# Kernel optimization log

Hardware: AMD Instinct MI355X
Metric: run time of the kernel (lower is better)

Reference implementation:

```python
import jax, jax.numpy as jnp
import numpy as np

FEAT = 256      # config.feature_size
HID = 256       # config.hidden_size
MAXC = 10       # config.max_child_num
NSEM = 64       # Tree.num_sem
B = 32768       # number of parent nodes (one batched tree level)


def _forward(box_input, eps, W_box, b_box, W1, b1, W2, b2,
             Ws1, bs1, Wmu, bmu, Wvar, bvar, sem_ids, n_children):
    # ---- BoxEncoder on every leaf child: relu(Linear(10 -> FEAT)) ----
    leaf = jax.nn.relu(jnp.einsum('bmi,if->bmf', box_input, W_box) + b_box)  # [B,M,FEAT]
    # ---- concat semantic one-hot per child ----
    sem = jax.nn.one_hot(sem_ids, NSEM, dtype=leaf.dtype)                    # [B,M,NSEM]
    child_feats = jnp.concatenate([leaf, sem], axis=-1)                      # [B,M,FEAT+NSEM]
    # ---- SymmetricChildEncoder ----
    feat = jax.nn.relu(jnp.einsum('bmf,fh->bmh', child_feats, W1) + b1)      # [B,M,HID]
    exists = (jnp.arange(MAXC) < n_children[:, None]).astype(feat.dtype)[..., None]  # [B,M,1]
    x = jnp.max(feat * exists, axis=1)                                       # [B,HID]
    parent_feat = jax.nn.relu(x @ W2 + b2)                                   # [B,FEAT]
    # ---- Sampler (variational, probabilistic) ----
    enc = jax.nn.relu(parent_feat @ Ws1 + bs1)                               # [B,HID]
    mu = enc @ Wmu + bmu                                                     # [B,FEAT]
    logvar = enc @ Wvar + bvar                                               # [B,FEAT]
    std = jnp.exp(0.5 * logvar)
    kld = 1.0 + logvar - mu * mu - jnp.exp(logvar)
    return jnp.concatenate([eps * std + mu, kld], axis=1)                    # [B,2*FEAT]


def setup_inputs() -> dict:
    key = jax.random.key(0)
    ks = jax.random.split(key, 16)
    def lin_w(k, fan_in, shape):
        return (jax.random.normal(k, shape, jnp.float32) / np.sqrt(fan_in)).astype(jnp.float32)
    return {
        'box_input': jax.random.normal(ks[0], (B, MAXC, 10), jnp.float32),
        'eps': jax.random.normal(ks[1], (B, FEAT), jnp.float32),
        'W_box': lin_w(ks[2], 10, (10, FEAT)),
        'b_box': jnp.zeros((FEAT,), jnp.float32),
        'W1': lin_w(ks[3], FEAT + NSEM, (FEAT + NSEM, HID)),
        'b1': jnp.zeros((HID,), jnp.float32),
        'W2': lin_w(ks[4], HID, (HID, FEAT)),
        'b2': jnp.zeros((FEAT,), jnp.float32),
        'Ws1': lin_w(ks[5], FEAT, (FEAT, HID)),
        'bs1': jnp.zeros((HID,), jnp.float32),
        'Wmu': lin_w(ks[6], HID, (HID, FEAT)),
        'bmu': jnp.zeros((FEAT,), jnp.float32),
        'Wvar': lin_w(ks[7], HID, (HID, FEAT)),
        'bvar': jnp.zeros((FEAT,), jnp.float32),
        'sem_ids': jax.random.randint(ks[8], (B, MAXC), 0, NSEM, jnp.int32),
        'n_children': jax.random.randint(ks[9], (B,), 1, MAXC + 1, jnp.int32),
    }


def reference(box_input, eps, W_box, b_box, W1, b1, W2, b2,
              Ws1, bs1, Wmu, bmu, Wvar, bvar, sem_ids, n_children):
    return _forward(box_input, eps, W_box, b_box, W1, b1, W2, b2,
                    Ws1, bs1, Wmu, bmu, Wvar, bvar, sem_ids, n_children)
```

## Files before the change

kernel.cpp:

```cpp
#include <hip/hip_runtime.h>
#include <math.h>


#define NPAR  32768
#define LDA1  328
#define LDA2  264
#define W1F_OFF   0
#define W2F_OFF   81920
#define WBX_OFF   (81920 + 4*65536)
#define XBUF_OFF  (WBX_OFF + 8192)

typedef _Float16 f16;
typedef _Float16 f16x8 __attribute__((ext_vector_type(8)));
typedef float    f32x4 __attribute__((ext_vector_type(4)));

__device__ __forceinline__ void async16(const void* g, void* l) {
    __builtin_amdgcn_global_load_lds((const __attribute__((address_space(1))) void*)g,
                                     (__attribute__((address_space(3))) void*)l, 16, 0, 0);
}
__device__ __forceinline__ f32x4 mfma16(f16x8 a, f16x8 b, f32x4 c) {
    return __builtin_amdgcn_mfma_f32_16x16x32_f16(a, b, c, 0, 0, 0);
}

__global__ void kconv(const float* __restrict__ W1, const float* __restrict__ W2,
                      const float* __restrict__ Ws1, const float* __restrict__ Wmu,
                      const float* __restrict__ Wvar, const float* __restrict__ Wbox,
                      f16* __restrict__ ws) {
    int idx = blockIdx.x * 256 + threadIdx.x;
    if (idx < 81920) {
        int j = idx & 7, lane = (idx >> 3) & 63, t = idx >> 9;
        int c = t % 10, n16 = t / 10;
        int k = c * 32 + (lane >> 4) * 8 + j;
        int n = n16 * 16 + (lane & 15);
        ws[idx] = (f16)W1[k * 256 + n];
    } else if (idx < WBX_OFF) {
        int r = idx - 81920;
        int wsel = r >> 16, r2 = r & 65535;
        const float* s = (wsel == 0) ? W2 : (wsel == 1) ? Ws1 : (wsel == 2) ? Wmu : Wvar;
        int j = r2 & 7, lane = (r2 >> 3) & 63, c = (r2 >> 9) & 7, n16 = r2 >> 12;
        int k = c * 32 + (lane >> 4) * 8 + j;
        int n = n16 * 16 + (lane & 15);
        ws[idx] = (f16)s[k * 256 + n];
    } else if (idx < XBUF_OFF) {
        int r = idx - WBX_OFF;
        int j = r & 7, lane = (r >> 3) & 63, n16 = r >> 9;
        int k = (lane >> 4) * 8 + j;
        int n = n16 * 16 + (lane & 15);
        ws[idx] = (f16)((k < 10) ? Wbox[k * 256 + n] : 0.f);
    }
}

__global__ __launch_bounds__(256, 2)
void k1(const float* __restrict__ box, const float* __restrict__ bbox,
        const float* __restrict__ b1, const int* __restrict__ sem,
        const int* __restrict__ nch, const f16* __restrict__ wsh,
        f16* __restrict__ xbuf) {
    __shared__ __align__(16) f16 lA[80 * LDA1];
    __shared__ int lnc[8];

    int tid = threadIdx.x, blk = blockIdx.x;
    int w = tid >> 6, lane = tid & 63, q = lane >> 4, r16 = lane & 15;
    const f16* w1f = wsh + W1F_OFF;
    const f16* wbxf = wsh + WBX_OFF;

    if (tid < 8) lnc[tid] = nch[blk * 8 + tid];

    float bbv[4], b1v[4];
    #pragma unroll
    for (int nt = 0; nt < 4; nt++) {
        int col = w * 64 + nt * 16 + r16;
        bbv[nt] = bbox[col];
        b1v[nt] = b1[col];
    }

    f32x4 acc[5][4];
    {
        f16x8 bb[4], ab[5];
        #pragma unroll
        for (int nt = 0; nt < 4; nt++)
            bb[nt] = *(const f16x8*)&wbxf[((w * 4 + nt) * 64 + lane) * 8];
        #pragma unroll
        for (int mt = 0; mt < 5; mt++) {
            const float* bp = box + (size_t)blk * 800 + (mt * 16 + r16) * 10;
            float v[8] = {0.f, 0.f, 0.f, 0.f, 0.f, 0.f, 0.f, 0.f};
            if (q == 0) {
                float2 t0 = *(const float2*)(bp + 0), t1 = *(const float2*)(bp + 2);
                float2 t2 = *(const float2*)(bp + 4), t3 = *(const float2*)(bp + 6);
                v[0] = t0.x; v[1] = t0.y; v[2] = t1.x; v[3] = t1.y;
                v[4] = t2.x; v[5] = t2.y; v[6] = t3.x; v[7] = t3.y;
            } else if (q == 1) {
                float2 t = *(const float2*)(bp + 8);
                v[0] = t.x; v[1] = t.y;
            }
            f16x8 t;
            #pragma unroll
            for (int j = 0; j < 8; j++) t[j] = (f16)v[j];
            ab[mt] = t;
        }
        #pragma unroll
        for (int mt = 0; mt < 5; mt++)
            #pragma unroll
            for (int nt = 0; nt < 4; nt++)
                acc[mt][nt] = mfma16(ab[mt], bb[nt], (f32x4){0.f, 0.f, 0.f, 0.f});
    }
    #pragma unroll
    for (int mt = 0; mt < 5; mt++) {
        #pragma unroll
        for (int i = 0; i < 4; i++) {
            int r = mt * 16 + q * 4 + i;
            int p = (r * 205) >> 11;
            int d = (r - 10 * p) * 8 + p;
            #pragma unroll
            for (int nt = 0; nt < 4; nt++) {
                int col = w * 64 + nt * 16 + r16;
                lA[d * LDA1 + col] = (f16)fmaxf(acc[mt][nt][i] + bbv[nt], 0.f);
            }
        }
    }
    if (tid < 80) {
        int p8 = tid & 7, m8 = tid >> 3;
        int sid = sem[blk * 80 + p8 * 10 + m8];
        f16x8 z = {(f16)0.f, (f16)0.f, (f16)0.f, (f16)0.f, (f16)0.f, (f16)0.f, (f16)0.f, (f16)0.f};
        #pragma unroll
        for (int j = 0; j < 8; j++) *(f16x8*)&lA[tid * LDA1 + 256 + j * 8] = z;
        lA[tid * LDA1 + 256 + sid] = (f16)1.f;
    }

    #pragma unroll
    for (int mt = 0; mt < 5; mt++)
        #pragma unroll
        for (int nt = 0; nt < 4; nt++) acc[mt][nt] = (f32x4){0.f, 0.f, 0.f, 0.f};

    f16x8 bs[3][4];
    auto loadB = [&](int c, int s) {
        #pragma unroll
        for (int nt = 0; nt < 4; nt++)
            bs[s][nt] = *(const f16x8*)&w1f[(((w * 4 + nt) * 10 + c) * 64 + lane) * 8];
    };
    loadB(0, 0); loadB(1, 1); loadB(2, 2);
    __syncthreads();
    #pragma unroll
    for (int c = 0; c < 10; c++) {
        f16x8 a[5];
        #pragma unroll
        for (int mt = 0; mt < 5; mt++)
            a[mt] = *(const f16x8*)&lA[(mt * 16 + r16) * LDA1 + c * 32 + q * 8];
        int s = c % 3;
        #pragma unroll
        for (int mt = 0; mt < 5; mt++)
            #pragma unroll
            for (int nt = 0; nt < 4; nt++) acc[mt][nt] = mfma16(a[mt], bs[s][nt], acc[mt][nt]);
        if (c + 3 < 10) loadB(c + 3, s);
    }

    int qh = q >> 1, qb = q & 1;
    int ncv[4];
    #pragma unroll
    for (int i = 0; i < 4; i++) ncv[i] = lnc[4 * qb + i];
    float pm[4][4];
    #pragma unroll
    for (int i = 0; i < 4; i++)
        #pragma unroll
        for (int nt = 0; nt < 4; nt++) pm[i][nt] = 0.f;
    #pragma unroll
    for (int mt = 0; mt < 5; mt++) {
        int m = 2 * mt + qh;
        #pragma unroll
        for (int i = 0; i < 4; i++) {
            bool live = m < ncv[i];
            #pragma unroll
            for (int nt = 0; nt < 4; nt++) {
                float v = fmaxf(acc[mt][nt][i] + b1v[nt], 0.f);
                pm[i][nt] = fmaxf(pm[i][nt], live ? v : 0.f);
            }
        }
    }
    #pragma unroll
    for (int i = 0; i < 4; i++)
        #pragma unroll
        for (int nt = 0; nt < 4; nt++)
            pm[i][nt] = fmaxf(pm[i][nt], __shfl_xor(pm[i][nt], 32, 64));
    if (q < 2) {
        #pragma unroll
        for (int i = 0; i < 4; i++) {
            size_t row = (size_t)blk * 8 + 4 * q + i;
            #pragma unroll
            for (int nt = 0; nt < 4; nt++)
                xbuf[row * LDA2 + w * 64 + nt * 16 + r16] = (f16)pm[i][nt];
        }
    }
}

__global__ __launch_bounds__(256, 2)
void k2(const f16* __restrict__ xbuf, const f16* __restrict__ wsh,
        const float* __restrict__ b2, const float* __restrict__ bs1,
        const float* __restrict__ bmu, const float* __restrict__ bvar,
        const float* __restrict__ eps, float* __restrict__ out) {
    __shared__ __align__(16) f16 actA[32 * LDA2];
    __shared__ __align__(16) f16 actB[32 * LDA2];

    int tid = threadIdx.x, blk = blockIdx.x;
    int w = tid >> 6, lane = tid & 63, q = lane >> 4, r16 = lane & 15;
    const f16* w2f   = wsh + W2F_OFF;
    const f16* ws1f  = w2f + 65536;
    const f16* wmuf  = w2f + 2 * 65536;
    const f16* wvarf = w2f + 3 * 65536;

    float b2v[4], bs1v[4], bmv[4], bvv[4];
    #pragma unroll
    for (int nt = 0; nt < 4; nt++) {
        int col = w * 64 + nt * 16 + r16;
        b2v[nt] = b2[col]; bs1v[nt] = bs1[col];
        bmv[nt] = bmu[col]; bvv[nt] = bvar[col];
    }

    {
        const char* src = (const char*)(xbuf + (size_t)blk * 32 * LDA2);
        #pragma unroll
        for (int j = 0; j < 5; j++) {
            int idx = tid + j * 256;
            if (idx < 1056) async16(src + idx * 16, (char*)actA + idx * 16);
        }
    }

    f32x4 acc[2][4];
    f16x8 bs[3][4];
    auto loadB = [&](const f16* wt, int c, int s) {
        #pragma unroll
        for (int nt = 0; nt < 4; nt++)
            bs[s][nt] = *(const f16x8*)&wt[(((w * 4 + nt) * 8 + c) * 64 + lane) * 8];
    };
    auto gemm = [&](const f16* A, const f16* wt) {
        #pragma unroll
        for (int mt = 0; mt < 2; mt++)
            #pragma unroll
            for (int nt = 0; nt < 4; nt++) acc[mt][nt] = (f32x4){0.f, 0.f, 0.f, 0.f};
        #pragma unroll
        for (int c = 0; c < 8; c++) {
            f16x8 a[2];
            #pragma unroll
            for (int mt = 0; mt < 2; mt++)
                a[mt] = *(const f16x8*)&A[(mt * 16 + r16) * LDA2 + c * 32 + q * 8];
            int s = c % 3;
            #pragma unroll
            for (int mt = 0; mt < 2; mt++)
                #pragma unroll
                for (int nt = 0; nt < 4; nt++) acc[mt][nt] = mfma16(a[mt], bs[s][nt], acc[mt][nt]);
            if (c + 3 < 8) loadB(wt, c + 3, s);
        }
    };

    loadB(w2f, 0, 0); loadB(w2f, 1, 1); loadB(w2f, 2, 2);
    __syncthreads();
    gemm(actA, w2f);
    #pragma unroll
    for (int nt = 0; nt < 4; nt++) {
        int col = w * 64 + nt * 16 + r16;
        #pragma unroll
        for (int mt = 0; mt < 2; mt++)
            #pragma unroll
            for (int i = 0; i < 4; i++)
                actB[(mt * 16 + q * 4 + i) * LDA2 + col] = (f16)fmaxf(acc[mt][nt][i] + b2v[nt], 0.f);
    }
    loadB(ws1f, 0, 0); loadB(ws1f, 1, 1); loadB(ws1f, 2, 2);
    __syncthreads();

    gemm(actB, ws1f);
    #pragma unroll
    for (int nt = 0; nt < 4; nt++) {
        int col = w * 64 + nt * 16 + r16;
        #pragma unroll
        for (int mt = 0; mt < 2; mt++)
            #pragma unroll
            for (int i = 0; i < 4; i++)
                actA[(mt * 16 + q * 4 + i) * LDA2 + col] = (f16)fmaxf(acc[mt][nt][i] + bs1v[nt], 0.f);
    }
    loadB(wmuf, 0, 0); loadB(wmuf, 1, 1); loadB(wmuf, 2, 2);
    __syncthreads();

    gemm(actA, wmuf);
    f32x4 mu[2][4];
    #pragma unroll
    for (int mt = 0; mt < 2; mt++)
        #pragma unroll
        for (int nt = 0; nt < 4; nt++) mu[mt][nt] = acc[mt][nt];

    float ev[2][4][4];
    #pragma unroll
    for (int mt = 0; mt < 2; mt++)
        #pragma unroll
        for (int i = 0; i < 4; i++) {
            size_t grow = (size_t)blk * 32 + mt * 16 + q * 4 + i;
            #pragma unroll
            for (int nt = 0; nt < 4; nt++)
                ev[mt][nt][i] = eps[grow * 256 + w * 64 + nt * 16 + r16];
        }

    loadB(wvarf, 0, 0); loadB(wvarf, 1, 1); loadB(wvarf, 2, 2);
    gemm(actA, wvarf);
    #pragma unroll
    for (int mt = 0; mt < 2; mt++)
        #pragma unroll
        for (int nt = 0; nt < 4; nt++) {
            int col = w * 64 + nt * 16 + r16;
            #pragma unroll
            for (int i = 0; i < 4; i++) {
                size_t grow = (size_t)blk * 32 + mt * 16 + q * 4 + i;
                float m_ = mu[mt][nt][i] + bmv[nt];
                float lv = acc[mt][nt][i] + bvv[nt];
                float e  = expf(lv);
                out[grow * 512 + col]       = ev[mt][nt][i] * sqrtf(e) + m_;
                out[grow * 512 + 256 + col] = 1.f + lv - m_ * m_ - e;
            }
        }
}

extern "C" void kernel_launch(void* const* d_in, const int* in_sizes, int n_in,
                              void* d_out, int out_size, void* d_ws, size_t ws_size,
                              hipStream_t stream) {
    const float* box  = (const float*)d_in[0];
    const float* eps  = (const float*)d_in[1];
    const float* Wbox = (const float*)d_in[2];
    const float* bbox = (const float*)d_in[3];
    const float* W1   = (const float*)d_in[4];
    const float* b1   = (const float*)d_in[5];
    const float* W2   = (const float*)d_in[6];
    const float* b2   = (const float*)d_in[7];
    const float* Ws1  = (const float*)d_in[8];
    const float* bs1  = (const float*)d_in[9];
    const float* Wmu  = (const float*)d_in[10];
    const float* bmu  = (const float*)d_in[11];
    const float* Wvar = (const float*)d_in[12];
    const float* bvar = (const float*)d_in[13];
    const int*   sem  = (const int*)d_in[14];
    const int*   nch  = (const int*)d_in[15];

    f16* wsh  = (f16*)d_ws;
    f16* xbuf = wsh + XBUF_OFF;

    kconv<<<XBUF_OFF / 256, 256, 0, stream>>>(W1, W2, Ws1, Wmu, Wvar, Wbox, wsh);
    k1<<<NPAR / 8, 256, 0, stream>>>(box, bbox, b1, sem, nch, wsh, xbuf);
    k2<<<NPAR / 32, 256, 0, stream>>>(xbuf, wsh, b2, bs1, bmu, bvar, eps, (float*)d_out);
}
```

Baseline: 218.8 us.

## Fuse child-encoder and sampler kernels, keep pooled features in LDS

Merges the two main kernels into one. Each block now loops over four 8-parent groups to build a 32-row pooled feature tile in shared memory, then runs the W2/Ws1/Wmu/Wvar GEMM chain on that tile directly. This removes the global xbuf round trip and one kernel launch. In exchange it cuts the grid to a quarter of the former k1 block count, serialises the four groups inside a block, and raises LDS use per block, which may lower occupancy.

```diff
diff --git a/kernel.cpp b/kernel.cpp
--- a/kernel.cpp
+++ b/kernel.cpp
@@ -8,16 +8,12 @@
 #define W1F_OFF   0
 #define W2F_OFF   81920
 #define WBX_OFF   (81920 + 4*65536)
-#define XBUF_OFF  (WBX_OFF + 8192)
+#define WS_END    (WBX_OFF + 8192)
 
 typedef _Float16 f16;
 typedef _Float16 f16x8 __attribute__((ext_vector_type(8)));
 typedef float    f32x4 __attribute__((ext_vector_type(4)));
 
-__device__ __forceinline__ void async16(const void* g, void* l) {
-    __builtin_amdgcn_global_load_lds((const __attribute__((address_space(1))) void*)g,
-                                     (__attribute__((address_space(3))) void*)l, 16, 0, 0);
-}
 __device__ __forceinline__ f32x4 mfma16(f16x8 a, f16x8 b, f32x4 c) {
     return __builtin_amdgcn_mfma_f32_16x16x32_f16(a, b, c, 0, 0, 0);
 }
@@ -41,7 +37,7 @@
         int k = c * 32 + (lane >> 4) * 8 + j;
         int n = n16 * 16 + (lane & 15);
         ws[idx] = (f16)s[k * 256 + n];
-    } else if (idx < XBUF_OFF) {
+    } else if (idx < WS_END) {
         int r = idx - WBX_OFF;
         int j = r & 7, lane = (r >> 3) & 63, n16 = r >> 9;
         int k = (lane >> 4) * 8 + j;
@@ -51,19 +47,20 @@
 }
 
 __global__ __launch_bounds__(256, 2)
-void k1(const float* __restrict__ box, const float* __restrict__ bbox,
+void kf(const float* __restrict__ box, const float* __restrict__ bbox,
         const float* __restrict__ b1, const int* __restrict__ sem,
         const int* __restrict__ nch, const f16* __restrict__ wsh,
-        f16* __restrict__ xbuf) {
+        const float* __restrict__ b2, const float* __restrict__ bs1,
+        const float* __restrict__ bmu, const float* __restrict__ bvar,
+        const float* __restrict__ eps, float* __restrict__ out) {
     __shared__ __align__(16) f16 lA[80 * LDA1];
+    __shared__ __align__(16) f16 xl[32 * LDA2];
     __shared__ int lnc[8];
 
     int tid = threadIdx.x, blk = blockIdx.x;
     int w = tid >> 6, lane = tid & 63, q = lane >> 4, r16 = lane & 15;
-    const f16* w1f = wsh + W1F_OFF;
+    const f16* w1f  = wsh + W1F_OFF;
     const f16* wbxf = wsh + WBX_OFF;
-
-    if (tid < 8) lnc[tid] = nch[blk * 8 + tid];
 
     float bbv[4], b1v[4];
     #pragma unroll
@@ -73,138 +70,137 @@
         b1v[nt] = b1[col];
     }
 
-    f32x4 acc[5][4];
-    {
-        f16x8 bb[4], ab[5];
-        #pragma unroll
-        for (int nt = 0; nt < 4; nt++)
-            bb[nt] = *(const f16x8*)&wbxf[((w * 4 + nt) * 64 + lane) * 8];
+    #pragma unroll 1
+    for (int t = 0; t < 4; t++) {
+        int g = blk * 4 + t;
+        if (t) __syncthreads();
+
+        if (tid < 8) lnc[tid] = nch[g * 8 + tid];
+
+        f32x4 acc[5][4];
+        {
+            f16x8 bb[4], ab[5];
+            #pragma unroll
+            for (int nt = 0; nt < 4; nt++)
+                bb[nt] = *(const f16x8*)&wbxf[((w * 4 + nt) * 64 + lane) * 8];
+            #pragma unroll
+            for (int mt = 0; mt < 5; mt++) {
+                const float* bp = box + (size_t)g * 800 + (mt * 16 + r16) * 10;
+                float v[8] = {0.f, 0.f, 0.f, 0.f, 0.f, 0.f, 0.f, 0.f};
+                if (q == 0) {
+                    float2 t0 = *(const float2*)(bp + 0), t1 = *(const float2*)(bp + 2);
+                    float2 t2 = *(const float2*)(bp + 4), t3 = *(const float2*)(bp + 6);
+                    v[0] = t0.x; v[1] = t0.y; v[2] = t1.x; v[3] = t1.y;
+                    v[4] = t2.x; v[5] = t2.y; v[6] = t3.x; v[7] = t3.y;
+                } else if (q == 1) {
+                    float2 tt = *(const float2*)(bp + 8);
+                    v[0] = tt.x; v[1] = tt.y;
+                }
+                f16x8 tv;
+                #pragma unroll
+                for (int j = 0; j < 8; j++) tv[j] = (f16)v[j];
+                ab[mt] = tv;
+            }
+            #pragma unroll
+            for (int mt = 0; mt < 5; mt++)
+                #pragma unroll
+                for (int nt = 0; nt < 4; nt++)
+                    acc[mt][nt] = mfma16(ab[mt], bb[nt], (f32x4){0.f, 0.f, 0.f, 0.f});
+        }
         #pragma unroll
         for (int mt = 0; mt < 5; mt++) {
-            const float* bp = box + (size_t)blk * 800 + (mt * 16 + r16) * 10;
-            float v[8] = {0.f, 0.f, 0.f, 0.f, 0.f, 0.f, 0.f, 0.f};
-            if (q == 0) {
-                float2 t0 = *(const float2*)(bp + 0), t1 = *(const float2*)(bp + 2);
-                float2 t2 = *(const float2*)(bp + 4), t3 = *(const float2*)(bp + 6);
-                v[0] = t0.x; v[1] = t0.y; v[2] = t1.x; v[3] = t1.y;
-                v[4] = t2.x; v[5] = t2.y; v[6] = t3.x; v[7] = t3.y;
-            } else if (q == 1) {
-                float2 t = *(const float2*)(bp + 8);
-                v[0] = t.x; v[1] = t.y;
-            }
-            f16x8 t;
-            #pragma unroll
-            for (int j = 0; j < 8; j++) t[j] = (f16)v[j];
-            ab[mt] = t;
-        }
+            #pragma unroll
+            for (int i = 0; i < 4; i++) {
+                int r = mt * 16 + q * 4 + i;
+                int p = (r * 205) >> 11;
+                int d = (r - 10 * p) * 8 + p;
+                #pragma unroll
+                for (int nt = 0; nt < 4; nt++) {
+                    int col = w * 64 + nt * 16 + r16;
+                    lA[d * LDA1 + col] = (f16)fmaxf(acc[mt][nt][i] + bbv[nt], 0.f);
+                }
+            }
+        }
+        if (tid < 80) {
+            int p8 = tid & 7, m8 = tid >> 3;
+            int sid = sem[g * 80 + p8 * 10 + m8];
+            f16x8 z = {(f16)0.f, (f16)0.f, (f16)0.f, (f16)0.f, (f16)0.f, (f16)0.f, (f16)0.f, (f16)0.f};
+            #pragma unroll
+            for (int j = 0; j < 8; j++) *(f16x8*)&lA[tid * LDA1 + 256 + j * 8] = z;
+            lA[tid * LDA1 + 256 + sid] = (f16)1.f;
+        }
+
         #pragma unroll
         for (int mt = 0; mt < 5; mt++)
             #pragma unroll
+            for (int nt = 0; nt < 4; nt++) acc[mt][nt] = (f32x4){0.f, 0.f, 0.f, 0.f};
+
+        f16x8 bs[3][4];
+        auto loadB = [&](int c, int s) {
+            #pragma unroll
             for (int nt = 0; nt < 4; nt++)
-                acc[mt][nt] = mfma16(ab[mt], bb[nt], (f32x4){0.f, 0.f, 0.f, 0.f});
-    }
-    #pragma unroll
-    for (int mt = 0; mt < 5; mt++) {
-        #pragma unroll
-        for (int i = 0; i < 4; i++) {
-            int r = mt * 16 + q * 4 + i;
-            int p = (r * 205) >> 11;
-            int d = (r - 10 * p) * 8 + p;
-            #pragma unroll
-            for (int nt = 0; nt < 4; nt++) {
-                int col = w * 64 + nt * 16 + r16;
-                lA[d * LDA1 + col] = (f16)fmaxf(acc[mt][nt][i] + bbv[nt], 0.f);
-            }
-        }
-    }
-    if (tid < 80) {
-        int p8 = tid & 7, m8 = tid >> 3;
-        int sid = sem[blk * 80 + p8 * 10 + m8];
-        f16x8 z = {(f16)0.f, (f16)0.f, (f16)0.f, (f16)0.f, (f16)0.f, (f16)0.f, (f16)0.f, (f16)0.f};
-        #pragma unroll
-        for (int j = 0; j < 8; j++) *(f16x8*)&lA[tid * LDA1 + 256 + j * 8] = z;
-        lA[tid * LDA1 + 256 + sid] = (f16)1.f;
-    }
-
-    #pragma unroll
-    for (int mt = 0; mt < 5; mt++)
-        #pragma unroll
-        for (int nt = 0; nt < 4; nt++) acc[mt][nt] = (f32x4){0.f, 0.f, 0.f, 0.f};
-
-    f16x8 bs[3][4];
-    auto loadB = [&](int c, int s) {
-        #pragma unroll
-        for (int nt = 0; nt < 4; nt++)
-            bs[s][nt] = *(const f16x8*)&w1f[(((w * 4 + nt) * 10 + c) * 64 + lane) * 8];
-    };
-    loadB(0, 0); loadB(1, 1); loadB(2, 2);
+                bs[s][nt] = *(const f16x8*)&w1f[(((w * 4 + nt) * 10 + c) * 64 + lane) * 8];
+        };
+        loadB(0, 0); loadB(1, 1); loadB(2, 2);
+        __syncthreads();
+        #pragma unroll
+        for (int c = 0; c < 10; c++) {
+            f16x8 a[5];
+            #pragma unroll
+            for (int mt = 0; mt < 5; mt++)
+                a[mt] = *(const f16x8*)&lA[(mt * 16 + r16) * LDA1 + c * 32 + q * 8];
+            int s = c % 3;
+            #pragma unroll
+            for (int mt = 0; mt < 5; mt++)
+                #pragma unroll
+                for (int nt = 0; nt < 4; nt++) acc[mt][nt] = mfma16(a[mt], bs[s][nt], acc[mt][nt]);
+            if (c + 3 < 10) loadB(c + 3, s);
+        }
+
+        int qh = q >> 1, qb = q & 1;
+        int ncv[4];
+        #pragma unroll
+        for (int i = 0; i < 4; i++) ncv[i] = lnc[4 * qb + i];
+        float pm[4][4];
+        #pragma unroll
+        for (int i = 0; i < 4; i++)
+            #pragma unroll
+            for (int nt = 0; nt < 4; nt++) pm[i][nt] = 0.f;
+        #pragma unroll
+        for (int mt = 0; mt < 5; mt++) {
+            int m = 2 * mt + qh;
+            #pragma unroll
+            for (int i = 0; i < 4; i++) {
+                bool live = m < ncv[i];
+                #pragma unroll
+                for (int nt = 0; nt < 4; nt++) {
+                    float v = fmaxf(acc[mt][nt][i] + b1v[nt], 0.f);
+                    pm[i][nt] = fmaxf(pm[i][nt], live ? v : 0.f);
+                }
+            }
+        }
+        #pragma unroll
+        for (int i = 0; i < 4; i++)
+            #pragma unroll
+            for (int nt = 0; nt < 4; nt++)
+                pm[i][nt] = fmaxf(pm[i][nt], __shfl_xor(pm[i][nt], 32, 64));
+        if (q < 2) {
+            #pragma unroll
+            for (int i = 0; i < 4; i++) {
+                int row = t * 8 + 4 * q + i;
+                #pragma unroll
+                for (int nt = 0; nt < 4; nt++)
+                    xl[row * LDA2 + w * 64 + nt * 16 + r16] = (f16)pm[i][nt];
+            }
+        }
+    }
     __syncthreads();
-    #pragma unroll
-    for (int c = 0; c < 10; c++) {
-        f16x8 a[5];
-        #pragma unroll
-        for (int mt = 0; mt < 5; mt++)
-            a[mt] = *(const f16x8*)&lA[(mt * 16 + r16) * LDA1 + c * 32 + q * 8];
-        int s = c % 3;
-        #pragma unroll
-        for (int mt = 0; mt < 5; mt++)
-            #pragma unroll
-            for (int nt = 0; nt < 4; nt++) acc[mt][nt] = mfma16(a[mt], bs[s][nt], acc[mt][nt]);
-        if (c + 3 < 10) loadB(c + 3, s);
-    }
-
-    int qh = q >> 1, qb = q & 1;
-    int ncv[4];
-    #pragma unroll
-    for (int i = 0; i < 4; i++) ncv[i] = lnc[4 * qb + i];
-    float pm[4][4];
-    #pragma unroll
-    for (int i = 0; i < 4; i++)
-        #pragma unroll
-        for (int nt = 0; nt < 4; nt++) pm[i][nt] = 0.f;
-    #pragma unroll
-    for (int mt = 0; mt < 5; mt++) {
-        int m = 2 * mt + qh;
-        #pragma unroll
-        for (int i = 0; i < 4; i++) {
-            bool live = m < ncv[i];
-            #pragma unroll
-            for (int nt = 0; nt < 4; nt++) {
-                float v = fmaxf(acc[mt][nt][i] + b1v[nt], 0.f);
-                pm[i][nt] = fmaxf(pm[i][nt], live ? v : 0.f);
-            }
-        }
-    }
-    #pragma unroll
-    for (int i = 0; i < 4; i++)
-        #pragma unroll
-        for (int nt = 0; nt < 4; nt++)
-            pm[i][nt] = fmaxf(pm[i][nt], __shfl_xor(pm[i][nt], 32, 64));
-    if (q < 2) {
-        #pragma unroll
-        for (int i = 0; i < 4; i++) {
-            size_t row = (size_t)blk * 8 + 4 * q + i;
-            #pragma unroll
-            for (int nt = 0; nt < 4; nt++)
-                xbuf[row * LDA2 + w * 64 + nt * 16 + r16] = (f16)pm[i][nt];
-        }
-    }
-}
-
-__global__ __launch_bounds__(256, 2)
-void k2(const f16* __restrict__ xbuf, const f16* __restrict__ wsh,
-        const float* __restrict__ b2, const float* __restrict__ bs1,
-        const float* __restrict__ bmu, const float* __restrict__ bvar,
-        const float* __restrict__ eps, float* __restrict__ out) {
-    __shared__ __align__(16) f16 actA[32 * LDA2];
-    __shared__ __align__(16) f16 actB[32 * LDA2];
-
-    int tid = threadIdx.x, blk = blockIdx.x;
-    int w = tid >> 6, lane = tid & 63, q = lane >> 4, r16 = lane & 15;
+
     const f16* w2f   = wsh + W2F_OFF;
     const f16* ws1f  = w2f + 65536;
     const f16* wmuf  = w2f + 2 * 65536;
     const f16* wvarf = w2f + 3 * 65536;
+    f16* actB = lA;
 
     float b2v[4], bs1v[4], bmv[4], bvv[4];
     #pragma unroll
@@ -214,18 +210,9 @@
         bmv[nt] = bmu[col]; bvv[nt] = bvar[col];
     }
 
-    {
-        const char* src = (const char*)(xbuf + (size_t)blk * 32 * LDA2);
-        #pragma unroll
-        for (int j = 0; j < 5; j++) {
-            int idx = tid + j * 256;
-            if (idx < 1056) async16(src + idx * 16, (char*)actA + idx * 16);
-        }
-    }
-
     f32x4 acc[2][4];
     f16x8 bs[3][4];
-    auto loadB = [&](const f16* wt, int c, int s) {
+    auto loadB2 = [&](const f16* wt, int c, int s) {
         #pragma unroll
         for (int nt = 0; nt < 4; nt++)
             bs[s][nt] = *(const f16x8*)&wt[(((w * 4 + nt) * 8 + c) * 64 + lane) * 8];
@@ -246,13 +233,12 @@
             for (int mt = 0; mt < 2; mt++)
                 #pragma unroll
                 for (int nt = 0; nt < 4; nt++) acc[mt][nt] = mfma16(a[mt], bs[s][nt], acc[mt][nt]);
-            if (c + 3 < 8) loadB(wt, c + 3, s);
+            if (c + 3 < 8) loadB2(wt, c + 3, s);
         }
     };
 
-    loadB(w2f, 0, 0); loadB(w2f, 1, 1); loadB(w2f, 2, 2);
-    __syncthreads();
-    gemm(actA, w2f);
+    loadB2(w2f, 0, 0); loadB2(w2f, 1, 1); loadB2(w2f, 2, 2);
+    gemm(xl, w2f);
     #pragma unroll
     for (int nt = 0; nt < 4; nt++) {
         int col = w * 64 + nt * 16 + r16;
@@ -262,7 +248,7 @@
             for (int i = 0; i < 4; i++)
                 actB[(mt * 16 + q * 4 + i) * LDA2 + col] = (f16)fmaxf(acc[mt][nt][i] + b2v[nt], 0.f);
     }
-    loadB(ws1f, 0, 0); loadB(ws1f, 1, 1); loadB(ws1f, 2, 2);
+    loadB2(ws1f, 0, 0); loadB2(ws1f, 1, 1); loadB2(ws1f, 2, 2);
     __syncthreads();
 
     gemm(actB, ws1f);
@@ -273,12 +259,12 @@
         for (int mt = 0; mt < 2; mt++)
             #pragma unroll
             for (int i = 0; i < 4; i++)
-                actA[(mt * 16 + q * 4 + i) * LDA2 + col] = (f16)fmaxf(acc[mt][nt][i] + bs1v[nt], 0.f);
-    }
-    loadB(wmuf, 0, 0); loadB(wmuf, 1, 1); loadB(wmuf, 2, 2);
+                xl[(mt * 16 + q * 4 + i) * LDA2 + col] = (f16)fmaxf(acc[mt][nt][i] + bs1v[nt], 0.f);
+    }
+    loadB2(wmuf, 0, 0); loadB2(wmuf, 1, 1); loadB2(wmuf, 2, 2);
     __syncthreads();
 
-    gemm(actA, wmuf);
+    gemm(xl, wmuf);
     f32x4 mu[2][4];
     #pragma unroll
     for (int mt = 0; mt < 2; mt++)
@@ -296,8 +282,8 @@
                 ev[mt][nt][i] = eps[grow * 256 + w * 64 + nt * 16 + r16];
         }
 
-    loadB(wvarf, 0, 0); loadB(wvarf, 1, 1); loadB(wvarf, 2, 2);
-    gemm(actA, wvarf);
+    loadB2(wvarf, 0, 0); loadB2(wvarf, 1, 1); loadB2(wvarf, 2, 2);
+    gemm(xl, wvarf);
     #pragma unroll
     for (int mt = 0; mt < 2; mt++)
         #pragma unroll
@@ -335,10 +321,9 @@
     const int*   sem  = (const int*)d_in[14];
     const int*   nch  = (const int*)d_in[15];
 
-    f16* wsh  = (f16*)d_ws;
-    f16* xbuf = wsh + XBUF_OFF;
-
-    kconv<<<XBUF_OFF / 256, 256, 0, stream>>>(W1, W2, Ws1, Wmu, Wvar, Wbox, wsh);
-    k1<<<NPAR / 8, 256, 0, stream>>>(box, bbox, b1, sem, nch, wsh, xbuf);
-    k2<<<NPAR / 32, 256, 0, stream>>>(xbuf, wsh, b2, bs1, bmu, bvar, eps, (float*)d_out);
+    f16* wsh = (f16*)d_ws;
+
+    kconv<<<WS_END / 256, 256, 0, stream>>>(W1, W2, Ws1, Wmu, Wvar, Wbox, wsh);
+    kf<<<NPAR / 32, 256, 0, stream>>>(box, bbox, b1, sem, nch, wsh,
+                                      b2, bs1, bmu, bvar, eps, (float*)d_out);
 }
```

Result: slower. 283.6 us (+29.6%).

## Stage k2 epilogue through LDS for coalesced vector eps loads and output stores

Applied to the files above, without the earlier changes.

The final mu/logvar tiles are staged through shared memory (reusing the activation buffers as fp32) in two 16-row halves, so each wave reads and writes full rows with 16-byte vector accesses for eps and the output. This replaces the scattered 4-byte per-lane global loads and stores from the MFMA fragment layout. It also removes the early eps prefetch into registers and raises the launch-bounds occupancy hint to 3 blocks per CU. The cost is extra LDS traffic and barriers, and eps is no longer loaded ahead of the final GEMM.

```diff
diff --git a/kernel.cpp b/kernel.cpp
--- a/kernel.cpp
+++ b/kernel.cpp
@@ -191,13 +191,16 @@
     }
 }
 
-__global__ __launch_bounds__(256, 2)
+__global__ __launch_bounds__(256, 3)
 void k2(const f16* __restrict__ xbuf, const f16* __restrict__ wsh,
         const float* __restrict__ b2, const float* __restrict__ bs1,
         const float* __restrict__ bmu, const float* __restrict__ bvar,
         const float* __restrict__ eps, float* __restrict__ out) {
-    __shared__ __align__(16) f16 actA[32 * LDA2];
-    __shared__ __align__(16) f16 actB[32 * LDA2];
+    __shared__ __align__(16) f16 sh[2 * 32 * LDA2];
+    f16* actA = sh;
+    f16* actB = sh + 32 * LDA2;
+    float* sh32 = (float*)sh;
+    const int LVW = 16 * 260;
 
     int tid = threadIdx.x, blk = blockIdx.x;
     int w = tid >> 6, lane = tid & 63, q = lane >> 4, r16 = lane & 15;
@@ -285,34 +288,42 @@
         #pragma unroll
         for (int nt = 0; nt < 4; nt++) mu[mt][nt] = acc[mt][nt];
 
-    float ev[2][4][4];
-    #pragma unroll
-    for (int mt = 0; mt < 2; mt++)
-        #pragma unroll
-        for (int i = 0; i < 4; i++) {
-            size_t grow = (size_t)blk * 32 + mt * 16 + q * 4 + i;
-            #pragma unroll
-            for (int nt = 0; nt < 4; nt++)
-                ev[mt][nt][i] = eps[grow * 256 + w * 64 + nt * 16 + r16];
-        }
-
     loadB(wvarf, 0, 0); loadB(wvarf, 1, 1); loadB(wvarf, 2, 2);
     gemm(actA, wvarf);
-    #pragma unroll
-    for (int mt = 0; mt < 2; mt++)
+    __syncthreads();
+
+    #pragma unroll
+    for (int h = 0; h < 2; h++) {
+        if (h) __syncthreads();
         #pragma unroll
         for (int nt = 0; nt < 4; nt++) {
             int col = w * 64 + nt * 16 + r16;
             #pragma unroll
             for (int i = 0; i < 4; i++) {
-                size_t grow = (size_t)blk * 32 + mt * 16 + q * 4 + i;
-                float m_ = mu[mt][nt][i] + bmv[nt];
-                float lv = acc[mt][nt][i] + bvv[nt];
-                float e  = expf(lv);
-                out[grow * 512 + col]       = ev[mt][nt][i] * sqrtf(e) + m_;
-                out[grow * 512 + 256 + col] = 1.f + lv - m_ * m_ - e;
-            }
-        }
+                int row16 = q * 4 + i;
+                sh32[row16 * 260 + col]       = mu[h][nt][i] + bmv[nt];
+                sh32[LVW + row16 * 260 + col] = acc[h][nt][i] + bvv[nt];
+            }
+        }
+        __syncthreads();
+        #pragma unroll
+        for (int j = 0; j < 4; j++) {
+            int row16 = 4 * j + w;
+            size_t grow = (size_t)blk * 32 + h * 16 + row16;
+            f32x4 m4 = *(const f32x4*)&sh32[row16 * 260 + lane * 4];
+            f32x4 l4 = *(const f32x4*)&sh32[LVW + row16 * 260 + lane * 4];
+            f32x4 e4 = *(const f32x4*)&eps[grow * 256 + lane * 4];
+            f32x4 o1, o2;
+            #pragma unroll
+            for (int i = 0; i < 4; i++) {
+                float e = expf(l4[i]);
+                o1[i] = e4[i] * sqrtf(e) + m4[i];
+                o2[i] = 1.f + l4[i] - m4[i] * m4[i] - e;
+            }
+            *(f32x4*)&out[grow * 512 + lane * 4]       = o1;
+            *(f32x4*)&out[grow * 512 + 256 + lane * 4] = o2;
+        }
+    }
 }
 
 extern "C" void kernel_launch(void* const* d_in, const int* in_sizes, int n_in,
```

After: 219.6 us. About the same (+0.4%).
